# Kernel tuning notes

Hardware: AMD Instinct MI355X
Metric: run time of the kernel (lower is better)

Reference implementation:

```python
import jax, jax.numpy as jnp
import numpy as np

BS, T, C, H, W = 2, 3, 256, 48, 48
NH, NP, NL = 8, 4, 3
DH = C // NH
HW = H * W
LQ = T * HW


def conv2d(x, w, b):
    # x: (N,C,H,W), w: (O,I,3,3), padding=1 (SAME)
    y = jax.lax.conv_general_dilated(x, w, (1, 1), 'SAME',
                                     dimension_numbers=('NCHW', 'OIHW', 'NCHW'))
    return y + b[None, :, None, None]


def grid_sample(img, grid, align_corners, padding_mode):
    # img: (B,C,Hi,Wi); grid: (B,Hg,Wg,2) in [-1,1], last dim = (x,y)
    B, Ch, Hi, Wi = img.shape
    gx, gy = grid[..., 0], grid[..., 1]
    if align_corners:
        x = (gx + 1.0) * 0.5 * (Wi - 1)
        y = (gy + 1.0) * 0.5 * (Hi - 1)
    else:
        x = ((gx + 1.0) * Wi - 1.0) * 0.5
        y = ((gy + 1.0) * Hi - 1.0) * 0.5
    if padding_mode == 'border':
        x = jnp.clip(x, 0.0, Wi - 1)
        y = jnp.clip(y, 0.0, Hi - 1)
    x0 = jnp.floor(x); y0 = jnp.floor(y)
    x1 = x0 + 1.0; y1 = y0 + 1.0
    wx1 = x - x0; wx0 = 1.0 - wx1
    wy1 = y - y0; wy0 = 1.0 - wy1
    imgf = img.reshape(B, Ch, Hi * Wi)

    def gather(xi, yi):
        xc = jnp.clip(xi, 0, Wi - 1).astype(jnp.int32)
        yc = jnp.clip(yi, 0, Hi - 1).astype(jnp.int32)
        flat = (yc * Wi + xc).reshape(B, 1, -1)
        g = jnp.take_along_axis(imgf, flat, axis=2).reshape(B, Ch, *xi.shape[1:])
        if padding_mode == 'zeros':
            valid = ((xi >= 0) & (xi <= Wi - 1) & (yi >= 0) & (yi <= Hi - 1))
            g = g * valid[:, None].astype(img.dtype)
        return g

    out = (gather(x0, y0) * (wx0 * wy0)[:, None]
           + gather(x1, y0) * (wx1 * wy0)[:, None]
           + gather(x0, y1) * (wx0 * wy1)[:, None]
           + gather(x1, y1) * (wx1 * wy1)[:, None])
    return out


def warp(x, flo):
    # x: (B,C,H,W), flo: (B,2,H,W) pixel flow; border padding, align_corners=True
    B, Ch, Hh, Ww = x.shape
    gy, gx = jnp.meshgrid(jnp.arange(Hh), jnp.arange(Ww), indexing='ij')
    grid = jnp.stack([gx, gy], 0).astype(x.dtype)[None]  # (1,2,H,W)
    v = grid + flo
    vx = 2.0 * v[:, 0] / max(Ww - 1, 1) - 1.0
    vy = 2.0 * v[:, 1] / max(Hh - 1, 1) - 1.0
    g = jnp.stack([vx, vy], -1)  # (B,H,W,2)
    return grid_sample(x, g, align_corners=True, padding_mode='border')


def flow_guid_offset(flow_forward, flow_backward, off, h, w):
    # off: (N, LQ, NH, NL, NP, 2) -> add frame-to-frame flows per (query level, key level)
    N = off.shape[0]
    hw = h * w
    off = off.reshape(N, NL, hw, NH, NL, NP, 2)
    f01 = flow_forward[:, 0]; f12 = flow_forward[:, 1]
    f02 = f01 + warp(f12, f01)
    b10 = flow_backward[:, 0]; b21 = flow_backward[:, 1]
    b20 = b21 + warp(b10, b21)

    def flat(f):
        return f.transpose(0, 2, 3, 1).reshape(N, hw, 2)

    f01, f12, f02, b10, b21, b20 = map(flat, (f01, f12, f02, b10, b21, b20))
    z = jnp.zeros_like(f01)
    add = jnp.stack([
        jnp.stack([z, f01, f02], axis=2),
        jnp.stack([b10, z, f12], axis=2),
        jnp.stack([b20, b21, z], axis=2)], axis=1)  # (N, 3, hw, 3, 2)
    off = off + add[:, :, :, None, :, None, :]
    return off.reshape(N, NL * hw, NH, NL, NP, 2)


def setup_inputs():
    key = jax.random.key(0)
    ks = jax.random.split(key, 12)
    query = jax.random.normal(ks[0], (BS, T, C, H, W), dtype=jnp.float32)
    input_flatten = jax.random.normal(ks[1], (BS, T, C, H, W), dtype=jnp.float32)
    reference_points = jax.random.uniform(ks[2], (BS, LQ, NL, 2), dtype=jnp.float32)
    input_spatial_shapes = jnp.array([[H, W]] * NL, dtype=jnp.int32)
    input_level_start_index = jnp.array([0, HW, 2 * HW], dtype=jnp.int32)
    input_padding_mask = jnp.zeros((BS, LQ), dtype=bool)
    flow_forward = 3.0 * jax.random.normal(ks[3], (BS, 2, 2, H, W), dtype=jnp.float32)
    flow_backward = 3.0 * jax.random.normal(ks[4], (BS, 2, 2, H, W), dtype=jnp.float32)
    # sampling_offsets bias init (as in _reset_parameters)
    thetas = np.arange(NH) * (2.0 * np.pi / NH)
    g = np.stack([np.cos(thetas), np.sin(thetas)], -1)
    g = g / np.abs(g).max(-1, keepdims=True)
    g = np.tile(g.reshape(NH, 1, 1, 2), (1, NL, NP, 1))
    g = g * (np.arange(NP) + 1).reshape(1, 1, NP, 1)
    b_off = jnp.asarray(g.reshape(-1), dtype=jnp.float32)
    fan = 1.0 / np.sqrt(C * 9)
    w_off = 0.01 * jax.random.normal(ks[5], (NH * NL * NP * 2, C, 3, 3), dtype=jnp.float32)
    w_attn = 0.01 * jax.random.normal(ks[6], (NH * NL * NP, C, 3, 3), dtype=jnp.float32)
    b_attn = jnp.zeros((NH * NL * NP,), dtype=jnp.float32)
    w_val = fan * jax.random.normal(ks[7], (C, C, 3, 3), dtype=jnp.float32)
    b_val = jnp.zeros((C,), dtype=jnp.float32)
    w_out = fan * jax.random.normal(ks[8], (C, C, 3, 3), dtype=jnp.float32)
    b_out = jnp.zeros((C,), dtype=jnp.float32)
    return {'query': query, 'reference_points': reference_points,
            'input_flatten': input_flatten,
            'input_spatial_shapes': input_spatial_shapes,
            'input_level_start_index': input_level_start_index,
            'input_padding_mask': input_padding_mask,
            'flow_forward': flow_forward, 'flow_backward': flow_backward,
            'w_off': w_off, 'b_off': b_off, 'w_attn': w_attn, 'b_attn': b_attn,
            'w_val': w_val, 'b_val': b_val, 'w_out': w_out, 'b_out': b_out}


def reference(query, reference_points, input_flatten, input_spatial_shapes,
              input_level_start_index, input_padding_mask, flow_forward,
              flow_backward, w_off, b_off, w_attn, b_attn, w_val, b_val,
              w_out, b_out):
    bs, t, c, h, w = query.shape
    q2d = query.reshape(bs * t, c, h, w)
    value = conv2d(input_flatten.reshape(bs * t, c, h, w), w_val, b_val)
    off = conv2d(q2d, w_off, b_off)
    attn = conv2d(q2d, w_attn, b_attn)

    def to_seq(x2d, ch):
        return x2d.reshape(bs, t, ch, h * w).transpose(0, 1, 3, 2).reshape(bs, t * h * w, ch)

    value = to_seq(value, c)
    off = to_seq(off, NH * NL * NP * 2)
    attn = to_seq(attn, NH * NL * NP)
    value = jnp.where(input_padding_mask[..., None], 0.0, value)
    value = value.reshape(bs, t * h * w, NH, DH)
    off = off.reshape(bs, LQ, NH, NL, NP, 2)
    off = flow_guid_offset(flow_forward, flow_backward, off, h, w)
    attn = jax.nn.softmax(attn.reshape(bs, LQ, NH, NL * NP), axis=-1)
    attn = attn.reshape(bs, LQ, NH, NL, NP)
    # offset normalizer: (W_l, H_l) per level
    norm = jnp.stack([input_spatial_shapes[:, 1], input_spatial_shapes[:, 0]], -1).astype(off.dtype)
    loc = reference_points[:, :, None, :, None, :] + off / norm[None, None, None, :, None, :]
    grids = 2.0 * loc - 1.0  # (bs, LQ, NH, NL, NP, 2)
    # values per level -> (NL*bs*NH, DH, h, w)
    v = value.reshape(bs, NL, h, w, NH, DH).transpose(1, 0, 4, 5, 2, 3).reshape(NL * bs * NH, DH, h, w)
    g = grids.transpose(3, 0, 2, 1, 4, 5).reshape(NL * bs * NH, LQ, NP, 2)
    sampled = grid_sample(v, g, align_corners=False, padding_mode='zeros')  # (NL*bs*NH, DH, LQ, NP)
    sampled = sampled.reshape(NL, bs, NH, DH, LQ, NP)
    out = jnp.einsum('lnhdqp,nqhlp->nqhd', sampled, attn).reshape(bs, LQ, c)
    out = out.reshape(bs, t, h * w, c).transpose(0, 1, 3, 2).reshape(bs * t, c, h, w)
    return conv2d(out, w_out, b_out)
```

## Files before the change

### kernel.cpp

```cpp
#include <hip/hip_runtime.h>
#include <hip/hip_bf16.h>

#define BS   2
#define T    3
#define CCH  256
#define HH   48
#define WW   48
#define NH   8
#define NP   4
#define NL   3
#define DH   32
#define HWP  (HH*WW)
#define LQ   (T*HWP)
#define NIMG (BS*T)

typedef short v8s __attribute__((ext_vector_type(8)));
typedef float v4f __attribute__((ext_vector_type(4)));
typedef float v2f __attribute__((ext_vector_type(2)));
typedef unsigned int v2u __attribute__((ext_vector_type(2)));

__device__ __forceinline__ unsigned short f2b(float f) {
    unsigned u = __float_as_uint(f);
    return (unsigned short)((u + 0x7FFFu + ((u >> 16) & 1u)) >> 16);
}

#define GLOAD_LDS16(gp, lp) \
    __builtin_amdgcn_global_load_lds((const __attribute__((address_space(1))) unsigned int*)(const void*)(gp), \
                                     (__attribute__((address_space(3))) unsigned int*)(void*)(lp), 16, 0, 0)

#define LDS_SLAB  32768
#define LDS_ZROW  69632
#define LDS_TOTAL 69760

__global__ __launch_bounds__(256) void flow_kernel(
    const float* __restrict__ ff, const float* __restrict__ fb,
    float* __restrict__ addb)
{
    int idx = blockIdx.x * 256 + threadIdx.x;
    if (idx >= BS * HWP) return;
    int n = idx / HWP, pix = idx % HWP;
    int y = pix / WW, x = pix % WW;

    auto F = [&](const float* base, int i, int c, int p) {
        return base[n * (2*2*HWP) + i * (2*HWP) + c * HWP + p];
    };

    float f01x = F(ff,0,0,pix), f01y = F(ff,0,1,pix);
    float f12x = F(ff,1,0,pix), f12y = F(ff,1,1,pix);
    float b10x = F(fb,0,0,pix), b10y = F(fb,0,1,pix);
    float b21x = F(fb,1,0,pix), b21y = F(fb,1,1,pix);

    auto bil = [&](const float* base, int i, float fx, float fy, float* ox, float* oy) {
        float vx = (float)x + fx;
        float vy = (float)y + fy;
        float gx = 2.0f * vx / (float)(WW - 1) - 1.0f;
        float gy = 2.0f * vy / (float)(HH - 1) - 1.0f;
        float px = (gx + 1.0f) * 0.5f * (float)(WW - 1);
        float py = (gy + 1.0f) * 0.5f * (float)(HH - 1);
        px = fminf(fmaxf(px, 0.0f), (float)(WW - 1));
        py = fminf(fmaxf(py, 0.0f), (float)(HH - 1));
        float x0f = floorf(px), y0f = floorf(py);
        float wx1 = px - x0f, wx0 = 1.0f - wx1;
        float wy1 = py - y0f, wy0 = 1.0f - wy1;
        int xi0 = (int)x0f, yi0 = (int)y0f;
        int xc0 = min(max(xi0, 0), WW-1), xc1 = min(max(xi0+1, 0), WW-1);
        int yc0 = min(max(yi0, 0), HH-1), yc1 = min(max(yi0+1, 0), HH-1);
        float r[2];
        #pragma unroll
        for (int c = 0; c < 2; ++c) {
            float v00 = F(base, i, c, yc0*WW + xc0);
            float v10 = F(base, i, c, yc0*WW + xc1);
            float v01 = F(base, i, c, yc1*WW + xc0);
            float v11 = F(base, i, c, yc1*WW + xc1);
            r[c] = v00*(wx0*wy0) + v10*(wx1*wy0) + v01*(wx0*wy1) + v11*(wx1*wy1);
        }
        *ox = r[0]; *oy = r[1];
    };

    float wfx, wfy; bil(ff, 1, f01x, f01y, &wfx, &wfy);
    float f02x = f01x + wfx, f02y = f01y + wfy;
    float wbx, wby; bil(fb, 0, b21x, b21y, &wbx, &wby);
    float b20x = b21x + wbx, b20y = b21y + wby;

    float* A = addb + n * (3*HWP*6) + pix * 6;
    const int TS = HWP * 6;
    A[0] = 0.f;   A[1] = 0.f;   A[2] = f01x; A[3] = f01y; A[4] = f02x; A[5] = f02y;
    A[TS+0] = b10x; A[TS+1] = b10y; A[TS+2] = 0.f; A[TS+3] = 0.f; A[TS+4] = f12x; A[TS+5] = f12y;
    A[2*TS+0] = b20x; A[2*TS+1] = b20y; A[2*TS+2] = b21x; A[2*TS+3] = b21y; A[2*TS+4] = 0.f; A[2*TS+5] = 0.f;
}

__global__ __launch_bounds__(256) void wcvt2_kernel(
    const float* __restrict__ s0, const float* __restrict__ s1,
    unsigned short* __restrict__ dst, int M0, int M1, int Mpad)
{
    int idx = blockIdx.x * 256 + threadIdx.x;
    if (idx >= 9 * Mpad * 256) return;
    int k  = idx / (Mpad * 256);
    int oc = (idx / 256) % Mpad;
    int ic = idx % 256;
    float v = (oc < M0) ? s0[((size_t)oc * 256 + ic) * 9 + k]
            : (oc < M1) ? s1[((size_t)(oc - M0) * 256 + ic) * 9 + k] : 0.f;
    dst[idx] = f2b(v);
}

__global__ __launch_bounds__(256) void tcvt_kernel(
    const float* __restrict__ src, unsigned short* __restrict__ dst)
{
    __shared__ float lds[32][33];
    int px0 = blockIdx.x * 32, ic0 = blockIdx.y * 32, img = blockIdx.z;
    int t = threadIdx.x;
    #pragma unroll
    for (int s = 0; s < 4; ++s) {
        int icl = (t >> 5) + s * 8, pxl = t & 31;
        lds[icl][pxl] = src[((size_t)img * 256 + ic0 + icl) * HWP + px0 + pxl];
    }
    __syncthreads();
    #pragma unroll
    for (int s = 0; s < 4; ++s) {
        int pxl = (t >> 5) + s * 8, icl = t & 31;
        dst[((size_t)img * HWP + px0 + pxl) * 256 + ic0 + icl] = f2b(lds[icl][pxl]);
    }
}

__global__ __launch_bounds__(256) void convbig(
    int phase,
    const unsigned short* __restrict__ in_a,
    const unsigned short* __restrict__ in_b,
    const unsigned short* __restrict__ Wb_a,
    const unsigned short* __restrict__ Wb_b,
    const float* __restrict__ bias_a,
    const float* __restrict__ bias_off,
    const float* __restrict__ bias_attn,
    unsigned short* __restrict__ Vout,
    float* __restrict__ offb,
    float* __restrict__ attnb,
    float* __restrict__ outp,
    const unsigned char* __restrict__ mask)
{
    __shared__ __align__(16) char lds[LDS_TOTAL];

    const int tid  = threadIdx.x;
    const int lane = tid & 63;
    const int wv   = tid >> 6;

    int b = blockIdx.x;
    int cls, mt, nt, img, Mpad;
    const unsigned short *inb, *Wb;
    if (phase == 0) {
        if (b < 216) { cls = 0; mt = b % 2; int r = b / 2; nt = r % 18; img = r / 18;
                       inb = in_a; Wb = Wb_a; Mpad = 256; }
        else { b -= 216; cls = 1; mt = b % 3; int r = b / 3; nt = r % 18; img = r / 18;
               inb = in_b; Wb = Wb_b; Mpad = 384; }
    } else { cls = 2; mt = b % 2; int r = b / 2; nt = r % 18; img = r / 18;
             inb = in_a; Wb = Wb_a; Mpad = 256; }

    const int oc0 = mt * 128;
    const int pxb = nt * 128;
    const char* inIc = (const char*)(inb + (size_t)img * HWP * 256);
    const char* Wbc  = (const char*)Wb;

    if (tid < 8) {
        v8s z;
        #pragma unroll
        for (int j = 0; j < 8; ++j) z[j] = 0;
        *(v8s*)(lds + LDS_ZROW + tid * 16) = z;
    }

    const int r0   = pxb / 48;
    const int rlo  = (r0 > 0) ? (r0 - 1) : 0;
    const int pxlo = rlo * 48;

    const int lrow8 = lane >> 3;
    const int lcol  = lane & 7;

    const int rowl = lane & 15;
    const int g    = lane >> 4;
    const int keyx = (rowl & 7) << 4;
    const int aoff0 = ((wv >> 1) * 64 + rowl) * 128;
    const int pxw   = pxb + (wv & 1) * 64;
    int ypx[4], xpx[4];
    #pragma unroll
    for (int p = 0; p < 4; ++p) {
        int px = pxw + p * 16 + rowl;
        ypx[p] = px / 48;
        xpx[p] = px % 48;
    }
    int ocr_[4];
    #pragma unroll
    for (int j = 0; j < 4; ++j) ocr_[j] = j * 32 + wv * 8 + lrow8;

    v4f acc[4][4];
    #pragma unroll
    for (int m = 0; m < 4; ++m)
        #pragma unroll
        for (int p = 0; p < 4; ++p)
            #pragma unroll
            for (int e = 0; e < 4; ++e) acc[m][p][e] = 0.f;

    for (int c = 0; c < 4; ++c) {
        const int ic0b = c * 128;

        #pragma unroll
        for (int rr = 0; rr < 9; ++rr) {
            int pe  = rr * 32 + wv * 8 + lrow8;
            int gpx = pxlo + pe;
            if (gpx > 2303) gpx = 2303;
            GLOAD_LDS16(inIc + (size_t)gpx * 512 + ic0b + ((lcol ^ (pe & 7)) << 4),
                        lds + LDS_SLAB + (rr * 32 + wv * 8) * 128);
        }
        #pragma unroll
        for (int j = 0; j < 4; ++j) {
            GLOAD_LDS16(Wbc + (size_t)(oc0 + ocr_[j]) * 512 + ic0b + ((lcol ^ (ocr_[j] & 7)) << 4),
                        lds + (j * 32 + wv * 8) * 128);
        }
        asm volatile("s_waitcnt vmcnt(0) lgkmcnt(0)" ::: "memory");
        __builtin_amdgcn_s_barrier();

        for (int k = 0; k < 9; ++k) {
            const int dy = k / 3 - 1, dx = k % 3 - 1;
            const int cur = k & 1;
            if (k < 8) {
                const char* wk1 = Wbc + (size_t)(k + 1) * Mpad * 512;
                #pragma unroll
                for (int j = 0; j < 4; ++j) {
                    GLOAD_LDS16(wk1 + (size_t)(oc0 + ocr_[j]) * 512 + ic0b + ((lcol ^ (ocr_[j] & 7)) << 4),
                                lds + (cur ^ 1) * 16384 + (j * 32 + wv * 8) * 128);
                }
                asm volatile("s_waitcnt vmcnt(4)" ::: "memory");
            } else {
                asm volatile("s_waitcnt vmcnt(0)" ::: "memory");
            }
            __builtin_amdgcn_s_barrier();

            int bbase[4], bkey[4];
            #pragma unroll
            for (int p = 0; p < 4; ++p) {
                int ys = ypx[p] + dy, xs = xpx[p] + dx;
                bool val = ((unsigned)ys < 48u) && ((unsigned)xs < 48u);
                int pe = ys * 48 + xs - pxlo;
                bbase[p] = val ? (LDS_SLAB + pe * 128) : LDS_ZROW;
                bkey[p]  = val ? ((pe & 7) << 4) : 0;
            }

            #pragma unroll
            for (int kk = 0; kk < 2; ++kk) {
                const int col = kk * 64 + g * 16;
                v8s a[4], bfr[4];
                #pragma unroll
                for (int m = 0; m < 4; ++m)
                    a[m] = *(const v8s*)(lds + cur * 16384 + aoff0 + m * 2048 + (col ^ keyx));
                #pragma unroll
                for (int p = 0; p < 4; ++p)
                    bfr[p] = *(const v8s*)(lds + bbase[p] + (col ^ bkey[p]));
                #pragma unroll
                for (int m = 0; m < 4; ++m)
                    #pragma unroll
                    for (int p = 0; p < 4; ++p)
                        acc[m][p] = __builtin_amdgcn_mfma_f32_16x16x32_bf16(a[m], bfr[p], acc[m][p], 0, 0, 0);
            }
            __builtin_amdgcn_s_barrier();
        }
    }

    const int n = img / T, t = img % T;
    const int ocw = oc0 + (wv >> 1) * 64;

    #pragma unroll
    for (int p = 0; p < 4; ++p) {
        const int px_f = pxw + p * 16 + rowl;
        const int q = t * HWP + px_f;
        bool mk = (cls == 0) ? (mask[n * LQ + q] != 0) : false;
        #pragma unroll
        for (int m = 0; m < 4; ++m) {
            const int oc_f = ocw + m * 16 + g * 4;
            if (cls == 0) {
                unsigned short o[4];
                #pragma unroll
                for (int r = 0; r < 4; ++r) {
                    float v = acc[m][p][r] + bias_a[oc_f + r];
                    if (mk) v = 0.f;
                    o[r] = f2b(v);
                }
                int head = oc_f >> 5, d0 = oc_f & 31;
                v2u pk;
                pk[0] = (unsigned)o[0] | ((unsigned)o[1] << 16);
                pk[1] = (unsigned)o[2] | ((unsigned)o[3] << 16);
                *(v2u*)(Vout + (((size_t)(t * BS + n) * NH + head) * HWP + px_f) * 32 + d0) = pk;
            } else if (cls == 1) {
                if (oc_f < 192) {
                    v4f v;
                    #pragma unroll
                    for (int r = 0; r < 4; ++r) v[r] = acc[m][p][r] + bias_off[oc_f + r];
                    *(v4f*)(offb + ((size_t)n * LQ + q) * 192 + oc_f) = v;
                } else if (oc_f < 288) {
                    v4f v;
                    #pragma unroll
                    for (int r = 0; r < 4; ++r) v[r] = acc[m][p][r] + bias_attn[oc_f - 192 + r];
                    *(v4f*)(attnb + ((size_t)n * LQ + q) * 96 + (oc_f - 192)) = v;
                }
            } else {
                #pragma unroll
                for (int r = 0; r < 4; ++r)
                    outp[((size_t)img * CCH + oc_f + r) * HWP + px_f] =
                        acc[m][p][r] + bias_a[oc_f + r];
            }
        }
    }
}

__global__ __launch_bounds__(256) void sample_kernel(
    const unsigned short* __restrict__ V,
    const float* __restrict__ offb,
    const float* __restrict__ attnb,
    const float* __restrict__ addb,
    const float* __restrict__ refp,
    unsigned short* __restrict__ midb)
{
    const int tid = threadIdx.x;
    const int gid = tid >> 3, li = tid & 7;
    const int pair = blockIdx.x * 32 + gid;
    const int head = pair & 7;
    const int nq = pair >> 3;
    const int n = nq / LQ, q = nq % LQ;
    const int t = q / HWP, pix = q % HWP;

    const float* al = attnb + ((size_t)n * LQ + q) * 96 + head * 12;
    float lg[12];
    {
        v4f t0 = *(const v4f*)al, t1 = *(const v4f*)(al + 4), t2 = *(const v4f*)(al + 8);
        #pragma unroll
        for (int j = 0; j < 4; ++j) { lg[j] = t0[j]; lg[4+j] = t1[j]; lg[8+j] = t2[j]; }
    }
    const float* ofp = offb + ((size_t)n * LQ + q) * 192 + head * 24;
    float of[24];
    #pragma unroll
    for (int j = 0; j < 6; ++j) {
        v4f v = *(const v4f*)(ofp + j * 4);
        #pragma unroll
        for (int e = 0; e < 4; ++e) of[j*4+e] = v[e];
    }
    const float* rpp = refp + ((size_t)n * LQ + q) * 6;
    const float* adp = addb + ((size_t)n * 3 * HWP + t * HWP + pix) * 6;
    float rp[6], ad[6];
    #pragma unroll
    for (int j = 0; j < 3; ++j) {
        v2f r = *(const v2f*)(rpp + j * 2);
        v2f a = *(const v2f*)(adp + j * 2);
        rp[j*2] = r[0]; rp[j*2+1] = r[1];
        ad[j*2] = a[0]; ad[j*2+1] = a[1];
    }

    float m = lg[0];
    #pragma unroll
    for (int j = 1; j < 12; ++j) m = fmaxf(m, lg[j]);
    float s = 0.f;
    #pragma unroll
    for (int j = 0; j < 12; ++j) { lg[j] = expf(lg[j] - m); s += lg[j]; }
    float inv = 1.0f / s;
    #pragma unroll
    for (int j = 0; j < 12; ++j) lg[j] *= inv;

    float acc0 = 0.f, acc1 = 0.f, acc2 = 0.f, acc3 = 0.f;

    #pragma unroll
    for (int l = 0; l < 3; ++l) {
        float refx = rp[l*2+0], refy = rp[l*2+1];
        float addx = ad[l*2+0], addy = ad[l*2+1];
        const unsigned short* Vi =
            V + (size_t)((l * BS + n) * NH + head) * HWP * DH + li * 4;
        #pragma unroll
        for (int p = 0; p < 4; ++p) {
            float ox = of[(l*4+p)*2+0] + addx;
            float oy = of[(l*4+p)*2+1] + addy;
            float locx = refx + ox * (1.0f/48.0f);
            float locy = refy + oy * (1.0f/48.0f);
            float gx = 2.0f*locx - 1.0f;
            float gy = 2.0f*locy - 1.0f;
            float pxf = ((gx + 1.0f) * 48.0f - 1.0f) * 0.5f;
            float pyf = ((gy + 1.0f) * 48.0f - 1.0f) * 0.5f;
            float x0f = floorf(pxf), y0f = floorf(pyf);
            float wx1 = pxf - x0f, wx0 = 1.0f - wx1;
            float wy1 = pyf - y0f, wy0 = 1.0f - wy1;
            int xi0 = (int)x0f, yi0 = (int)y0f;
            bool vx0 = (x0f >= 0.0f)     && (x0f <= 47.0f);
            bool vx1 = (x0f+1.f >= 0.0f) && (x0f+1.f <= 47.0f);
            bool vy0 = (y0f >= 0.0f)     && (y0f <= 47.0f);
            bool vy1 = (y0f+1.f >= 0.0f) && (y0f+1.f <= 47.0f);
            int xc0 = min(max(xi0, 0), 47),   xc1 = min(max(xi0+1, 0), 47);
            int yc0 = min(max(yi0, 0), 47),   yc1 = min(max(yi0+1, 0), 47);
            float aw = lg[l*4+p];
            float w00 = (vx0 && vy0) ? wx0*wy0*aw : 0.f;
            float w10 = (vx1 && vy0) ? wx1*wy0*aw : 0.f;
            float w01 = (vx0 && vy1) ? wx0*wy1*aw : 0.f;
            float w11 = (vx1 && vy1) ? wx1*wy1*aw : 0.f;
            v2u u00 = *(const v2u*)(Vi + (yc0*WW + xc0)*DH);
            v2u u10 = *(const v2u*)(Vi + (yc0*WW + xc1)*DH);
            v2u u01 = *(const v2u*)(Vi + (yc1*WW + xc0)*DH);
            v2u u11 = *(const v2u*)(Vi + (yc1*WW + xc1)*DH);
            #pragma unroll
            for (int c = 0; c < 4; ++c) {
                v2u u = (c == 0) ? u00 : (c == 1) ? u10 : (c == 2) ? u01 : u11;
                float w = (c == 0) ? w00 : (c == 1) ? w10 : (c == 2) ? w01 : w11;
                float f0 = __uint_as_float(u[0] << 16);
                float f1 = __uint_as_float(u[0] & 0xFFFF0000u);
                float f2 = __uint_as_float(u[1] << 16);
                float f3 = __uint_as_float(u[1] & 0xFFFF0000u);
                acc0 += w * f0; acc1 += w * f1; acc2 += w * f2; acc3 += w * f3;
            }
        }
    }

    unsigned short o0 = f2b(acc0), o1 = f2b(acc1), o2 = f2b(acc2), o3 = f2b(acc3);
    v2u pk;
    pk[0] = (unsigned)o0 | ((unsigned)o1 << 16);
    pk[1] = (unsigned)o2 | ((unsigned)o3 << 16);
    *(v2u*)(midb + ((size_t)(n * T + t) * HWP + pix) * 256 + head * 32 + li * 4) = pk;
}

extern "C" void kernel_launch(void* const* d_in, const int* in_sizes, int n_in,
                              void* d_out, int out_size, void* d_ws, size_t ws_size,
                              hipStream_t stream) {
    const float* query  = (const float*)d_in[0];
    const float* refp   = (const float*)d_in[1];
    const float* inputf = (const float*)d_in[2];
    const unsigned char* mask = (const unsigned char*)d_in[5];
    const float* ff     = (const float*)d_in[6];
    const float* fb     = (const float*)d_in[7];
    const float* w_off  = (const float*)d_in[8];
    const float* b_off  = (const float*)d_in[9];
    const float* w_attn = (const float*)d_in[10];
    const float* b_attn = (const float*)d_in[11];
    const float* w_val  = (const float*)d_in[12];
    const float* b_val  = (const float*)d_in[13];
    const float* w_out  = (const float*)d_in[14];
    const float* b_out  = (const float*)d_in[15];

    char* w = (char*)d_ws;
    float* offb  = (float*)w;           w += (size_t)BS*LQ*192*4;
    float* attnb = (float*)w;           w += (size_t)BS*LQ*96*4;
    float* addb  = (float*)w;           w += (size_t)BS*3*HWP*6*4;
    unsigned short* V      = (unsigned short*)w; w += (size_t)48*HWP*DH*2;
    unsigned short* inb_q  = (unsigned short*)w; w += (size_t)NIMG*HWP*256*2;
    unsigned short* inb_v  = (unsigned short*)w; w += (size_t)NIMG*HWP*256*2;
    unsigned short* midb   = inb_v;
    unsigned short* Wb_val = (unsigned short*)w; w += (size_t)9*256*256*2;
    unsigned short* Wb_oa  = (unsigned short*)w; w += (size_t)9*384*256*2;
    unsigned short* Wb_out = (unsigned short*)w; w += (size_t)9*256*256*2;
    float* outp = (float*)d_out;

    flow_kernel<<<(BS*HWP + 255)/256, 256, 0, stream>>>(ff, fb, addb);
    wcvt2_kernel<<<9*256, 256, 0, stream>>>(w_val, w_val, Wb_val, 256, 256, 256);
    wcvt2_kernel<<<9*384, 256, 0, stream>>>(w_off, w_attn, Wb_oa, 192, 288, 384);
    wcvt2_kernel<<<9*256, 256, 0, stream>>>(w_out, w_out, Wb_out, 256, 256, 256);
    tcvt_kernel<<<dim3(HWP/32, 8, NIMG), 256, 0, stream>>>(inputf, inb_v);
    tcvt_kernel<<<dim3(HWP/32, 8, NIMG), 256, 0, stream>>>(query,  inb_q);

    convbig<<<540, 256, 0, stream>>>(0, inb_v, inb_q, Wb_val, Wb_oa,
                                     b_val, b_off, b_attn,
                                     V, offb, attnb, nullptr, mask);

    sample_kernel<<<(BS*LQ*NH)/32, 256, 0, stream>>>(V, offb, attnb, addb, refp, midb);

    convbig<<<216, 256, 0, stream>>>(1, midb, nullptr, Wb_out, nullptr,
                                     b_out, nullptr, nullptr,
                                     nullptr, nullptr, nullptr, outp, nullptr);
}
```

Baseline: 156.8 us.

## Split final conv along input channels and drop weight double-buffering to shrink LDS

The output 3x3 conv is split into two halves over input-channel chunks, launching twice as many blocks. Each half writes an fp32 partial to workspace, and a new reduce kernel sums the halves and adds the bias. Separately, the per-tap weight tile is no longer double-buffered in LDS: each tap is loaded and then synchronised before use. This cuts the LDS footprint so more blocks can be resident per CU, in every conv launch. The cost is lost overlap of weight loads with MFMA work, extra barriers, and extra global traffic for the partial buffers and the reduction pass.

```diff
diff --git a/kernel.cpp b/kernel.cpp
--- a/kernel.cpp
+++ b/kernel.cpp
@@ -28,9 +28,11 @@
     __builtin_amdgcn_global_load_lds((const __attribute__((address_space(1))) unsigned int*)(const void*)(gp), \
                                      (__attribute__((address_space(3))) unsigned int*)(void*)(lp), 16, 0, 0)
 
-#define LDS_SLAB  32768
-#define LDS_ZROW  69632
-#define LDS_TOTAL 69760
+#define LDS_SLAB  16384
+#define LDS_ZROW  53248
+#define LDS_TOTAL 53376
+
+#define PBLK (NIMG*CCH*HWP)
 
 __global__ __launch_bounds__(256) void flow_kernel(
     const float* __restrict__ ff, const float* __restrict__ fb,
@@ -144,15 +146,20 @@
     const int wv   = tid >> 6;
 
     int b = blockIdx.x;
-    int cls, mt, nt, img, Mpad;
+    int cls, mt, nt, img, Mpad, c_lo, c_hi, s;
     const unsigned short *inb, *Wb;
     if (phase == 0) {
+        s = 0; c_lo = 0; c_hi = 4;
         if (b < 216) { cls = 0; mt = b % 2; int r = b / 2; nt = r % 18; img = r / 18;
                        inb = in_a; Wb = Wb_a; Mpad = 256; }
         else { b -= 216; cls = 1; mt = b % 3; int r = b / 3; nt = r % 18; img = r / 18;
                inb = in_b; Wb = Wb_b; Mpad = 384; }
-    } else { cls = 2; mt = b % 2; int r = b / 2; nt = r % 18; img = r / 18;
-             inb = in_a; Wb = Wb_a; Mpad = 256; }
+    } else {
+        cls = 3; s = b / 216; b = b % 216;
+        c_lo = 2 * s; c_hi = c_lo + 2;
+        mt = b % 2; int r = b / 2; nt = r % 18; img = r / 18;
+        inb = in_a; Wb = Wb_a; Mpad = 256;
+    }
 
     const int oc0 = mt * 128;
     const int pxb = nt * 128;
@@ -197,9 +204,10 @@
             #pragma unroll
             for (int e = 0; e < 4; ++e) acc[m][p][e] = 0.f;
 
-    for (int c = 0; c < 4; ++c) {
+    for (int c = c_lo; c < c_hi; ++c) {
         const int ic0b = c * 128;
 
+        __syncthreads();
         #pragma unroll
         for (int rr = 0; rr < 9; ++rr) {
             int pe  = rr * 32 + wv * 8 + lrow8;
@@ -208,30 +216,18 @@
             GLOAD_LDS16(inIc + (size_t)gpx * 512 + ic0b + ((lcol ^ (pe & 7)) << 4),
                         lds + LDS_SLAB + (rr * 32 + wv * 8) * 128);
         }
-        #pragma unroll
-        for (int j = 0; j < 4; ++j) {
-            GLOAD_LDS16(Wbc + (size_t)(oc0 + ocr_[j]) * 512 + ic0b + ((lcol ^ (ocr_[j] & 7)) << 4),
-                        lds + (j * 32 + wv * 8) * 128);
-        }
-        asm volatile("s_waitcnt vmcnt(0) lgkmcnt(0)" ::: "memory");
-        __builtin_amdgcn_s_barrier();
 
         for (int k = 0; k < 9; ++k) {
+            if (k) __syncthreads();
+            const char* wk = Wbc + (size_t)k * Mpad * 512;
+            #pragma unroll
+            for (int j = 0; j < 4; ++j) {
+                GLOAD_LDS16(wk + (size_t)(oc0 + ocr_[j]) * 512 + ic0b + ((lcol ^ (ocr_[j] & 7)) << 4),
+                            lds + (j * 32 + wv * 8) * 128);
+            }
+            __syncthreads();
+
             const int dy = k / 3 - 1, dx = k % 3 - 1;
-            const int cur = k & 1;
-            if (k < 8) {
-                const char* wk1 = Wbc + (size_t)(k + 1) * Mpad * 512;
-                #pragma unroll
-                for (int j = 0; j < 4; ++j) {
-                    GLOAD_LDS16(wk1 + (size_t)(oc0 + ocr_[j]) * 512 + ic0b + ((lcol ^ (ocr_[j] & 7)) << 4),
-                                lds + (cur ^ 1) * 16384 + (j * 32 + wv * 8) * 128);
-                }
-                asm volatile("s_waitcnt vmcnt(4)" ::: "memory");
-            } else {
-                asm volatile("s_waitcnt vmcnt(0)" ::: "memory");
-            }
-            __builtin_amdgcn_s_barrier();
-
             int bbase[4], bkey[4];
             #pragma unroll
             for (int p = 0; p < 4; ++p) {
@@ -248,7 +244,7 @@
                 v8s a[4], bfr[4];
                 #pragma unroll
                 for (int m = 0; m < 4; ++m)
-                    a[m] = *(const v8s*)(lds + cur * 16384 + aoff0 + m * 2048 + (col ^ keyx));
+                    a[m] = *(const v8s*)(lds + aoff0 + m * 2048 + (col ^ keyx));
                 #pragma unroll
                 for (int p = 0; p < 4; ++p)
                     bfr[p] = *(const v8s*)(lds + bbase[p] + (col ^ bkey[p]));
@@ -258,7 +254,6 @@
                     for (int p = 0; p < 4; ++p)
                         acc[m][p] = __builtin_amdgcn_mfma_f32_16x16x32_bf16(a[m], bfr[p], acc[m][p], 0, 0, 0);
             }
-            __builtin_amdgcn_s_barrier();
         }
     }
 
@@ -299,13 +294,30 @@
                     *(v4f*)(attnb + ((size_t)n * LQ + q) * 96 + (oc_f - 192)) = v;
                 }
             } else {
+                float* pb = outp + (size_t)s * PBLK;
                 #pragma unroll
                 for (int r = 0; r < 4; ++r)
-                    outp[((size_t)img * CCH + oc_f + r) * HWP + px_f] =
-                        acc[m][p][r] + bias_a[oc_f + r];
+                    pb[((size_t)img * CCH + oc_f + r) * HWP + px_f] = acc[m][p][r];
             }
         }
     }
+}
+
+__global__ __launch_bounds__(256) void reduce_kernel(
+    const float* __restrict__ part, const float* __restrict__ bias,
+    float* __restrict__ out)
+{
+    int i4 = blockIdx.x * 256 + threadIdx.x;
+    size_t i = (size_t)i4 * 4;
+    if (i >= (size_t)PBLK) return;
+    int oc = (int)((i / HWP) % CCH);
+    v4f a = *(const v4f*)(part + i);
+    v4f b = *(const v4f*)(part + PBLK + i);
+    float bv = bias[oc];
+    v4f o;
+    #pragma unroll
+    for (int e = 0; e < 4; ++e) o[e] = a[e] + b[e] + bv;
+    *(v4f*)(out + i) = o;
 }
 
 __global__ __launch_bounds__(256) void sample_kernel(
@@ -446,6 +458,7 @@
     unsigned short* Wb_val = (unsigned short*)w; w += (size_t)9*256*256*2;
     unsigned short* Wb_oa  = (unsigned short*)w; w += (size_t)9*384*256*2;
     unsigned short* Wb_out = (unsigned short*)w; w += (size_t)9*256*256*2;
+    float* partial = (float*)d_ws;
     float* outp = (float*)d_out;
 
     flow_kernel<<<(BS*HWP + 255)/256, 256, 0, stream>>>(ff, fb, addb);
@@ -461,7 +474,9 @@
 
     sample_kernel<<<(BS*LQ*NH)/32, 256, 0, stream>>>(V, offb, attnb, addb, refp, midb);
 
-    convbig<<<216, 256, 0, stream>>>(1, midb, nullptr, Wb_out, nullptr,
-                                     b_out, nullptr, nullptr,
-                                     nullptr, nullptr, nullptr, outp, nullptr);
-}
+    convbig<<<432, 256, 0, stream>>>(1, midb, nullptr, Wb_out, nullptr,
+                                     nullptr, nullptr, nullptr,
+                                     nullptr, nullptr, nullptr, partial, nullptr);
+
+    reduce_kernel<<<(PBLK/4 + 255)/256, 256, 0, stream>>>(partial, b_out, outp);
+}
```

Result: slower. 218.7 us (+39.5%).
